# Optimization experiments

Measured on AMD Instinct MI355X. Metric: run time of the kernel, lower is better.

## Reference

```python
import jax, jax.numpy as jnp
import numpy as np

B, T, I, H = 64, 1024, 128, 256

def setup_inputs() -> dict:
    key = jax.random.key(0)
    ks = jax.random.split(key, 9)
    std = 1.0 / np.sqrt(H)
    u = lambda k, shape: jax.random.uniform(k, shape, jnp.float32, -std, std)
    return {
        "x": jax.random.normal(ks[0], (B, T, I), jnp.float32),
        # layer 0: concat dim = I + H
        "Wf1": u(ks[1], (I + H, H)), "bf1": u(ks[2], (H,)),
        "Wc1": u(ks[3], (I + H, H)), "bc1": u(ks[4], (H,)),
        # layer 1: concat dim = H + H
        "Wf2": u(ks[5], (H + H, H)), "bf2": u(ks[6], (H,)),
        "Wc2": u(ks[7], (H + H, H)), "bc2": u(ks[8], (H,)),
    }

def _mgu_layer(x_seq, Wf, bf, Wc, bc):
    # x_seq: [B, T, D] -> outputs [B, T, H], final hidden [B, H]
    h0 = jnp.zeros((x_seq.shape[0], H), x_seq.dtype)
    def step(h, x_t):
        comb = jnp.concatenate([x_t, h], axis=-1)      # [B, D+H]
        f = jax.nn.sigmoid(comb @ Wf + bf)             # forget gate
        c = jnp.tanh(comb @ Wc + bc)                   # candidate
        h_new = f * h + (1.0 - f) * c
        return h_new, h_new
    hT, ys = jax.lax.scan(step, h0, jnp.swapaxes(x_seq, 0, 1))  # ys: [T, B, H]
    return jnp.swapaxes(ys, 0, 1), hT

def reference(x, Wf1, bf1, Wc1, bc1, Wf2, bf2, Wc2, bc2):
    y1, h1 = _mgu_layer(x, Wf1, bf1, Wc1, bc1)
    y2, h2 = _mgu_layer(y1, Wf2, bf2, Wc2, bc2)
    hidden = jnp.stack([h1, h2])  # [num_layers, B, H]
    return y2, hidden
```

## Files before the change

### kernel.cpp

```cpp
#include <hip/hip_runtime.h>

typedef unsigned int uint;
typedef _Float16 f16;
typedef _Float16 f16x2 __attribute__((ext_vector_type(2)));
typedef _Float16 f16x4 __attribute__((ext_vector_type(4)));
typedef _Float16 f16x8 __attribute__((ext_vector_type(8)));
typedef float f32x4 __attribute__((ext_vector_type(4)));

#define B_ 64
#define T_ 1024
#define I_ 128
#define H_ 256

template<int KIN>
__global__ void prep_wxt(const float* __restrict__ Wf, const float* __restrict__ Wc,
                         f16* __restrict__ WxT) {
  int o = blockIdx.x * 256 + threadIdx.x;
  if (o >= 512 * KIN) return;
  int n = o / KIN, k = o % KIN;
  float v = (n < 256) ? Wf[k * H_ + n] : Wc[k * H_ + (n - 256)];
  WxT[o] = (f16)v;
}

__global__ void prep_ut(const float* __restrict__ Wf, const float* __restrict__ Wc,
                        f16* __restrict__ UT, int DIN) {
  int o = blockIdx.x * 256 + threadIdx.x;
  int n = o >> 8, k = o & 255;
  const float* W = (n < 256) ? Wf : Wc;
  UT[o] = (f16)W[(DIN + k) * H_ + (n & 255)];
}

__global__ void init_sync(int* s) { if (threadIdx.x < 132) s[threadIdx.x] = 0; }

template<int KFULL, bool AF32>
__global__ __launch_bounds__(256) void gemm_xpart(const void* __restrict__ Av,
    const f16* __restrict__ Bt, const float* __restrict__ bf, const float* __restrict__ bc,
    f16* __restrict__ Xg) {
  __shared__ __align__(16) f16 As[128][72];
  __shared__ __align__(16) f16 Bs[128][72];
  const int m0 = blockIdx.x * 128, n0 = blockIdx.y * 128;
  const int tid = threadIdx.x, lane = tid & 63, wid = tid >> 6;
  const int wr = wid >> 1, wc = wid & 1;
  f32x4 zero4 = {0.f, 0.f, 0.f, 0.f};
  f32x4 acc[4][4];
  #pragma unroll
  for (int i = 0; i < 4; ++i)
    #pragma unroll
    for (int j = 0; j < 4; ++j) acc[i][j] = zero4;
  const int r2 = tid >> 1, hh = tid & 1;
  for (int kb = 0; kb < KFULL / 64; ++kb) {
    const int k0 = kb * 64;
    if (kb) __syncthreads();
    if (AF32) {
      const float* A = (const float*)Av;
      const float* src = A + (size_t)(m0 + r2) * KFULL + k0 + hh * 32;
      #pragma unroll
      for (int i = 0; i < 8; ++i) {
        float4 v = *(const float4*)(src + i * 4);
        f16x4 p = { (f16)v.x, (f16)v.y, (f16)v.z, (f16)v.w };
        *(f16x4*)&As[r2][hh * 32 + i * 4] = p;
      }
    } else {
      const f16* A = (const f16*)Av;
      const f16* src = A + (size_t)(m0 + r2) * KFULL + k0 + hh * 32;
      #pragma unroll
      for (int i = 0; i < 4; ++i)
        *(uint4*)&As[r2][hh * 32 + i * 8] = *(const uint4*)(src + i * 8);
    }
    {
      const f16* src = Bt + (size_t)(n0 + r2) * KFULL + k0 + hh * 32;
      #pragma unroll
      for (int i = 0; i < 4; ++i)
        *(uint4*)&Bs[r2][hh * 32 + i * 8] = *(const uint4*)(src + i * 8);
    }
    __syncthreads();
    #pragma unroll
    for (int kt = 0; kt < 2; ++kt) {
      f16x8 af[4], bfr[4];
      #pragma unroll
      for (int i = 0; i < 4; ++i)
        af[i] = *(const f16x8*)&As[wr * 64 + i * 16 + (lane & 15)][kt * 32 + (lane >> 4) * 8];
      #pragma unroll
      for (int j = 0; j < 4; ++j)
        bfr[j] = *(const f16x8*)&Bs[wc * 64 + j * 16 + (lane & 15)][kt * 32 + (lane >> 4) * 8];
      #pragma unroll
      for (int i = 0; i < 4; ++i)
        #pragma unroll
        for (int j = 0; j < 4; ++j)
          acc[i][j] = __builtin_amdgcn_mfma_f32_16x16x32_f16(af[i], bfr[j], acc[i][j], 0, 0, 0);
    }
  }
  const float* bias = (n0 < 256) ? bf : bc;
  #pragma unroll
  for (int j = 0; j < 4; ++j) {
    const int gn = n0 + wc * 64 + j * 16 + (lane & 15);
    const float bv = bias[gn & 255];
    #pragma unroll
    for (int i = 0; i < 4; ++i) {
      #pragma unroll
      for (int reg = 0; reg < 4; ++reg) {
        const int gm = m0 + wr * 64 + i * 16 + (lane >> 4) * 4 + reg;
        Xg[(size_t)gm * 512 + gn] = (f16)(acc[i][j][reg] + bv);
      }
    }
  }
}

__device__ __forceinline__ void gemm_tile_l2(const f16* __restrict__ A,
    const f16* __restrict__ Bt, const float* __restrict__ bf, const float* __restrict__ bc,
    f16* __restrict__ Xg, int m0, int n0, f16 (*As)[72], f16 (*Bs)[72]) {
  const int tid = threadIdx.x, lane = tid & 63, wid = tid >> 6;
  const bool act = tid < 256;
  f32x4 zero4 = {0.f, 0.f, 0.f, 0.f};
  f32x4 acc[2][2];
  #pragma unroll
  for (int i = 0; i < 2; ++i)
    #pragma unroll
    for (int j = 0; j < 2; ++j) acc[i][j] = zero4;
  const int arow = tid >> 3, aq = tid & 7;
  const int r2 = (tid & 255) >> 1, hh = tid & 1;
  for (int kb = 0; kb < 4; ++kb) {
    const int k0 = kb * 64;
    if (kb) __syncthreads();
    if (act) {
      const f16* srcA = A + (size_t)(m0 + arow) * 256 + k0 + aq * 8;
      *(uint4*)&As[arow][aq * 8] = *(const uint4*)srcA;
      const f16* srcB = Bt + (size_t)(n0 + r2) * 256 + k0 + hh * 32;
      #pragma unroll
      for (int i = 0; i < 4; ++i)
        *(uint4*)&Bs[r2][hh * 32 + i * 8] = *(const uint4*)(srcB + i * 8);
    }
    __syncthreads();
    if (wid < 4) {
      #pragma unroll
      for (int kt = 0; kt < 2; ++kt) {
        f16x8 af[2], bfr[2];
        #pragma unroll
        for (int i = 0; i < 2; ++i)
          af[i] = *(const f16x8*)&As[i * 16 + (lane & 15)][kt * 32 + (lane >> 4) * 8];
        #pragma unroll
        for (int j = 0; j < 2; ++j)
          bfr[j] = *(const f16x8*)&Bs[wid * 32 + j * 16 + (lane & 15)][kt * 32 + (lane >> 4) * 8];
        #pragma unroll
        for (int i = 0; i < 2; ++i)
          #pragma unroll
          for (int j = 0; j < 2; ++j)
            acc[i][j] = __builtin_amdgcn_mfma_f32_16x16x32_f16(af[i], bfr[j], acc[i][j], 0, 0, 0);
      }
    }
  }
  if (wid < 4) {
    const float* bias = (n0 < 256) ? bf : bc;
    #pragma unroll
    for (int j = 0; j < 2; ++j) {
      const int gn = n0 + wid * 32 + j * 16 + (lane & 15);
      const float bv = bias[gn & 255];
      #pragma unroll
      for (int i = 0; i < 2; ++i) {
        #pragma unroll
        for (int reg = 0; reg < 4; ++reg) {
          const int gm = m0 + i * 16 + (lane >> 4) * 4 + reg;
          Xg[(size_t)gm * 512 + gn] = (f16)(acc[i][j][reg] + bv);
        }
      }
    }
  }
  __syncthreads();
}

__device__ __forceinline__ void rec_core(const f16* __restrict__ UT,
    f16* __restrict__ Xg, float* __restrict__ yf, f16* __restrict__ yh,
    float* __restrict__ hid, const int g, int* prog_pub, int* done_gate,
    f16 (*hbuf)[16][264]) {
  const int tid = threadIdx.x;
  const int lane = tid & 63, w = tid >> 6;
  const int lr = lane & 15, lg = lane >> 4;
  const int m0 = g * 16;

  const int nt[4] = { 32 * w, 32 * w + 16, 256 + 32 * w, 256 + 32 * w + 16 };

  f16x8 uw[4][8];
  #pragma unroll
  for (int tt = 0; tt < 4; ++tt)
    #pragma unroll
    for (int kf = 0; kf < 8; ++kf)
      uw[tt][kf] = *(const f16x8*)&UT[(size_t)(nt[tt] + lr) * 256 + kf * 32 + lg * 8];
  #pragma unroll
  for (int tt = 0; tt < 4; ++tt)
    #pragma unroll
    for (int kf = 0; kf < 8; ++kf)
      asm volatile("" : "+v"(uw[tt][kf]));

  {
    uint* hz = (uint*)&hbuf[0][0][0];
    for (int i = tid; i < 2112; i += 512) hz[i] = 0u;
  }

  if (done_gate) {
    if (tid == 0)
      while (__hip_atomic_load(&done_gate[0], __ATOMIC_ACQUIRE, __HIP_MEMORY_SCOPE_AGENT) < 64)
        __builtin_amdgcn_s_sleep(8);
    __syncthreads();
  }

  const f16* xp[4];
  #pragma unroll
  for (int tt = 0; tt < 4; ++tt)
    xp[tt] = Xg + ((size_t)(m0 + lr) * T_) * 512 + nt[tt] + 4 * lg;

  float hreg[2][4] = {{0.f,0.f,0.f,0.f},{0.f,0.f,0.f,0.f}};
  f16x4 xcur[4];
  #pragma unroll
  for (int tt = 0; tt < 4; ++tt) xcur[tt] = *(const f16x4*)xp[tt];

  const size_t ybase = (size_t)(m0 + lr) * T_ * H_;
  const int ycol0 = 32 * w + 4 * lg;

  __syncthreads();

  #pragma unroll 1
  for (int t = 0; t < T_; ++t) {
    if (done_gate) {
      const int tp1 = t + 1;
      if ((tp1 & 31) == 0 && (tp1 >> 5) < 32) {
        if (tid == 0)
          while (__hip_atomic_load(&done_gate[tp1 >> 5], __ATOMIC_ACQUIRE, __HIP_MEMORY_SCOPE_AGENT) < 64)
            __builtin_amdgcn_s_sleep(8);
        __syncthreads();
      }
    }

    const int tn = (t + 1 < T_) ? t + 1 : t;
    f16x4 xn[4];
    #pragma unroll
    for (int tt = 0; tt < 4; ++tt) xn[tt] = *(const f16x4*)(xp[tt] + (size_t)tn * 512);

    const f16* hrow = &hbuf[t & 1][lr][0];
    f16x8 hf[8];
    #pragma unroll
    for (int kf = 0; kf < 8; ++kf)
      hf[kf] = *(const f16x8*)(hrow + kf * 32 + lg * 8);

    f32x4 acc[4];
    #pragma unroll
    for (int tt = 0; tt < 4; ++tt) acc[tt] = (f32x4){0.f, 0.f, 0.f, 0.f};
    #pragma unroll
    for (int kf = 0; kf < 8; ++kf)
      #pragma unroll
      for (int tt = 0; tt < 4; ++tt)
        acc[tt] = __builtin_amdgcn_mfma_f32_16x16x32_f16(uw[tt][kf], hf[kf], acc[tt], 0, 0, 0);

    f16x4 hn4[2];
    #pragma unroll
    for (int p = 0; p < 2; ++p) {
      #pragma unroll
      for (int r = 0; r < 4; ++r) {
        float pf = acc[p][r]     + (float)xcur[p][r];
        float pc = acc[2 + p][r] + (float)xcur[2 + p][r];
        float fg = __builtin_amdgcn_rcpf(1.f + __expf(-pf));
        float e2 = __expf(2.f * pc);
        float cc = 1.f - 2.f * __builtin_amdgcn_rcpf(e2 + 1.f);
        float hn = cc + fg * (hreg[p][r] - cc);
        hreg[p][r] = hn;
        hn4[p][r] = (f16)hn;
      }
      *(f16x4*)&hbuf[(t + 1) & 1][lr][ycol0 + 16 * p] = hn4[p];
    }
    if (yh) {
      #pragma unroll
      for (int p = 0; p < 2; ++p)
        *(f16x4*)(yh + ybase + (size_t)t * H_ + ycol0 + 16 * p) = hn4[p];
    }
    if (yf) {
      #pragma unroll
      for (int p = 0; p < 2; ++p) {
        float4 yv = make_float4(hreg[p][0], hreg[p][1], hreg[p][2], hreg[p][3]);
        *(float4*)(yf + ybase + (size_t)t * H_ + ycol0 + 16 * p) = yv;
      }
    }
    if (t == T_ - 1) {
      #pragma unroll
      for (int p = 0; p < 2; ++p) {
        float4 hv = make_float4(hreg[p][0], hreg[p][1], hreg[p][2], hreg[p][3]);
        *(float4*)(hid + (size_t)(m0 + lr) * H_ + ycol0 + 16 * p) = hv;
      }
    }

    asm volatile("s_waitcnt lgkmcnt(0)" ::: "memory");
    __builtin_amdgcn_s_barrier();
    asm volatile("" ::: "memory");

    if (prog_pub && ((t & 31) == 31)) {
      asm volatile("s_waitcnt vmcnt(0)" ::: "memory");
      __syncthreads();
      if (tid == 0)
        __hip_atomic_store(prog_pub, t + 1, __ATOMIC_RELEASE, __HIP_MEMORY_SCOPE_AGENT);
    }

    #pragma unroll
    for (int tt = 0; tt < 4; ++tt) xcur[tt] = xn[tt];
  }
}

__global__ __launch_bounds__(512, 1) void fused(const f16* __restrict__ UT1,
    const f16* __restrict__ UT2, f16* __restrict__ Xg, const f16* __restrict__ Wx2T,
    const float* __restrict__ bf2, const float* __restrict__ bc2,
    f16* __restrict__ y1h, float* __restrict__ y2,
    float* __restrict__ hid1, float* __restrict__ hid2, int* __restrict__ sync) {
  __shared__ __align__(16) f16 hbuf[2][16][264];
  __shared__ __align__(16) f16 As[32][72];
  __shared__ __align__(16) f16 Bs[128][72];
  int* prog = sync;
  int* done = sync + 4;
  const int bid = blockIdx.x, tid = threadIdx.x;

  if (bid < 4) {
    rec_core(UT1, Xg, nullptr, y1h, hid1, bid, &prog[bid], nullptr, hbuf);
  } else if (bid < 68) {
    const int wk = bid - 4;
    for (int j = 0; j < 128; ++j) {
      const int tau = wk + 64 * j;
      const int c = tau >> 8, rem = tau & 255, b = rem >> 2, n = rem & 3;
      const int g1 = b >> 4;
      if (tid == 0)
        while (__hip_atomic_load(&prog[g1], __ATOMIC_ACQUIRE, __HIP_MEMORY_SCOPE_AGENT) < c * 32 + 32)
          __builtin_amdgcn_s_sleep(8);
      __syncthreads();
      gemm_tile_l2(y1h, Wx2T, bf2, bc2, Xg, b * 1024 + c * 32, n * 128, As, Bs);
      asm volatile("s_waitcnt vmcnt(0)" ::: "memory");
      __syncthreads();
      if (tid == 0)
        __hip_atomic_fetch_add(&done[g1 * 32 + c], 1, __ATOMIC_ACQ_REL, __HIP_MEMORY_SCOPE_AGENT);
    }
  } else {
    const int g = bid - 68;
    rec_core(UT2, Xg, y2, nullptr, hid2, g, nullptr, &done[g * 32], hbuf);
  }
}

extern "C" void kernel_launch(void* const* d_in, const int* in_sizes, int n_in,
                              void* d_out, int out_size, void* d_ws, size_t ws_size,
                              hipStream_t stream) {
  (void)in_sizes; (void)n_in; (void)out_size; (void)ws_size;
  const float* x   = (const float*)d_in[0];
  const float* Wf1 = (const float*)d_in[1];
  const float* bf1 = (const float*)d_in[2];
  const float* Wc1 = (const float*)d_in[3];
  const float* bc1 = (const float*)d_in[4];
  const float* Wf2 = (const float*)d_in[5];
  const float* bf2 = (const float*)d_in[6];
  const float* Wc2 = (const float*)d_in[7];
  const float* bc2 = (const float*)d_in[8];
  float* out = (float*)d_out;

  char* ws = (char*)d_ws;
  f16*  Xg   = (f16*)(ws);
  f16*  y1h  = (f16*)(ws + 67108864);
  f16*  Wx1T = (f16*)(ws + 100663296);
  f16*  Wx2T = (f16*)(ws + 100794368);
  f16*  UT1  = (f16*)(ws + 101056512);
  f16*  UT2  = (f16*)(ws + 101318656);
  int*  sync = (int*)(ws + 101580800);

  float* y2   = out;
  float* hid1 = out + (size_t)B_ * T_ * H_;
  float* hid2 = hid1 + (size_t)B_ * H_;

  prep_wxt<128><<<256, 256, 0, stream>>>(Wf1, Wc1, Wx1T);
  prep_wxt<256><<<512, 256, 0, stream>>>(Wf2, Wc2, Wx2T);
  prep_ut<<<512, 256, 0, stream>>>(Wf1, Wc1, UT1, 128);
  prep_ut<<<512, 256, 0, stream>>>(Wf2, Wc2, UT2, 256);
  init_sync<<<1, 256, 0, stream>>>(sync);

  gemm_xpart<128, true ><<<dim3(512, 4), 256, 0, stream>>>(x, Wx1T, bf1, bc1, Xg);
  fused<<<72, 512, 0, stream>>>(UT1, UT2, Xg, Wx2T, bf2, bc2, y1h, y2, hid1, hid2, sync);
}
```

Measured before the change: 1.795 ms.

## Fold weight prep and layer-1 input GEMM into the persistent fused kernel

```diff
diff --git a/kernel.cpp b/kernel.cpp
--- a/kernel.cpp
+++ b/kernel.cpp
@@ -2,7 +2,6 @@
 
 typedef unsigned int uint;
 typedef _Float16 f16;
-typedef _Float16 f16x2 __attribute__((ext_vector_type(2)));
 typedef _Float16 f16x4 __attribute__((ext_vector_type(4)));
 typedef _Float16 f16x8 __attribute__((ext_vector_type(8)));
 typedef float f32x4 __attribute__((ext_vector_type(4)));
@@ -11,102 +10,10 @@
 #define T_ 1024
 #define I_ 128
 #define H_ 256
-
-template<int KIN>
-__global__ void prep_wxt(const float* __restrict__ Wf, const float* __restrict__ Wc,
-                         f16* __restrict__ WxT) {
-  int o = blockIdx.x * 256 + threadIdx.x;
-  if (o >= 512 * KIN) return;
-  int n = o / KIN, k = o % KIN;
-  float v = (n < 256) ? Wf[k * H_ + n] : Wc[k * H_ + (n - 256)];
-  WxT[o] = (f16)v;
-}
-
-__global__ void prep_ut(const float* __restrict__ Wf, const float* __restrict__ Wc,
-                        f16* __restrict__ UT, int DIN) {
-  int o = blockIdx.x * 256 + threadIdx.x;
-  int n = o >> 8, k = o & 255;
-  const float* W = (n < 256) ? Wf : Wc;
-  UT[o] = (f16)W[(DIN + k) * H_ + (n & 255)];
-}
-
-__global__ void init_sync(int* s) { if (threadIdx.x < 132) s[threadIdx.x] = 0; }
-
-template<int KFULL, bool AF32>
-__global__ __launch_bounds__(256) void gemm_xpart(const void* __restrict__ Av,
-    const f16* __restrict__ Bt, const float* __restrict__ bf, const float* __restrict__ bc,
-    f16* __restrict__ Xg) {
-  __shared__ __align__(16) f16 As[128][72];
-  __shared__ __align__(16) f16 Bs[128][72];
-  const int m0 = blockIdx.x * 128, n0 = blockIdx.y * 128;
-  const int tid = threadIdx.x, lane = tid & 63, wid = tid >> 6;
-  const int wr = wid >> 1, wc = wid & 1;
-  f32x4 zero4 = {0.f, 0.f, 0.f, 0.f};
-  f32x4 acc[4][4];
-  #pragma unroll
-  for (int i = 0; i < 4; ++i)
-    #pragma unroll
-    for (int j = 0; j < 4; ++j) acc[i][j] = zero4;
-  const int r2 = tid >> 1, hh = tid & 1;
-  for (int kb = 0; kb < KFULL / 64; ++kb) {
-    const int k0 = kb * 64;
-    if (kb) __syncthreads();
-    if (AF32) {
-      const float* A = (const float*)Av;
-      const float* src = A + (size_t)(m0 + r2) * KFULL + k0 + hh * 32;
-      #pragma unroll
-      for (int i = 0; i < 8; ++i) {
-        float4 v = *(const float4*)(src + i * 4);
-        f16x4 p = { (f16)v.x, (f16)v.y, (f16)v.z, (f16)v.w };
-        *(f16x4*)&As[r2][hh * 32 + i * 4] = p;
-      }
-    } else {
-      const f16* A = (const f16*)Av;
-      const f16* src = A + (size_t)(m0 + r2) * KFULL + k0 + hh * 32;
-      #pragma unroll
-      for (int i = 0; i < 4; ++i)
-        *(uint4*)&As[r2][hh * 32 + i * 8] = *(const uint4*)(src + i * 8);
-    }
-    {
-      const f16* src = Bt + (size_t)(n0 + r2) * KFULL + k0 + hh * 32;
-      #pragma unroll
-      for (int i = 0; i < 4; ++i)
-        *(uint4*)&Bs[r2][hh * 32 + i * 8] = *(const uint4*)(src + i * 8);
-    }
-    __syncthreads();
-    #pragma unroll
-    for (int kt = 0; kt < 2; ++kt) {
-      f16x8 af[4], bfr[4];
-      #pragma unroll
-      for (int i = 0; i < 4; ++i)
-        af[i] = *(const f16x8*)&As[wr * 64 + i * 16 + (lane & 15)][kt * 32 + (lane >> 4) * 8];
-      #pragma unroll
-      for (int j = 0; j < 4; ++j)
-        bfr[j] = *(const f16x8*)&Bs[wc * 64 + j * 16 + (lane & 15)][kt * 32 + (lane >> 4) * 8];
-      #pragma unroll
-      for (int i = 0; i < 4; ++i)
-        #pragma unroll
-        for (int j = 0; j < 4; ++j)
-          acc[i][j] = __builtin_amdgcn_mfma_f32_16x16x32_f16(af[i], bfr[j], acc[i][j], 0, 0, 0);
-    }
-  }
-  const float* bias = (n0 < 256) ? bf : bc;
-  #pragma unroll
-  for (int j = 0; j < 4; ++j) {
-    const int gn = n0 + wc * 64 + j * 16 + (lane & 15);
-    const float bv = bias[gn & 255];
-    #pragma unroll
-    for (int i = 0; i < 4; ++i) {
-      #pragma unroll
-      for (int reg = 0; reg < 4; ++reg) {
-        const int gm = m0 + wr * 64 + i * 16 + (lane >> 4) * 4 + reg;
-        Xg[(size_t)gm * 512 + gn] = (f16)(acc[i][j][reg] + bv);
-      }
-    }
-  }
-}
-
-__device__ __forceinline__ void gemm_tile_l2(const f16* __restrict__ A,
+#define NWK 64
+
+template<int KA, bool AF32>
+__device__ __forceinline__ void gemm_tile(const void* __restrict__ Av,
     const f16* __restrict__ Bt, const float* __restrict__ bf, const float* __restrict__ bc,
     f16* __restrict__ Xg, int m0, int n0, f16 (*As)[72], f16 (*Bs)[72]) {
   const int tid = threadIdx.x, lane = tid & 63, wid = tid >> 6;
@@ -119,13 +26,22 @@
     for (int j = 0; j < 2; ++j) acc[i][j] = zero4;
   const int arow = tid >> 3, aq = tid & 7;
   const int r2 = (tid & 255) >> 1, hh = tid & 1;
-  for (int kb = 0; kb < 4; ++kb) {
+  for (int kb = 0; kb < KA / 64; ++kb) {
     const int k0 = kb * 64;
     if (kb) __syncthreads();
     if (act) {
-      const f16* srcA = A + (size_t)(m0 + arow) * 256 + k0 + aq * 8;
-      *(uint4*)&As[arow][aq * 8] = *(const uint4*)srcA;
-      const f16* srcB = Bt + (size_t)(n0 + r2) * 256 + k0 + hh * 32;
+      if (AF32) {
+        const float* srcA = (const float*)Av + (size_t)(m0 + arow) * KA + k0 + aq * 8;
+        float4 v0 = *(const float4*)srcA;
+        float4 v1 = *(const float4*)(srcA + 4);
+        f16x8 p = { (f16)v0.x, (f16)v0.y, (f16)v0.z, (f16)v0.w,
+                    (f16)v1.x, (f16)v1.y, (f16)v1.z, (f16)v1.w };
+        *(f16x8*)&As[arow][aq * 8] = p;
+      } else {
+        const f16* srcA = (const f16*)Av + (size_t)(m0 + arow) * KA + k0 + aq * 8;
+        *(uint4*)&As[arow][aq * 8] = *(const uint4*)srcA;
+      }
+      const f16* srcB = Bt + (size_t)(n0 + r2) * KA + k0 + hh * 32;
       #pragma unroll
       for (int i = 0; i < 4; ++i)
         *(uint4*)&Bs[r2][hh * 32 + i * 8] = *(const uint4*)(srcB + i * 8);
@@ -168,10 +84,11 @@
   __syncthreads();
 }
 
-__device__ __forceinline__ void rec_core(const f16* __restrict__ UT,
+__device__ __forceinline__ void rec_core(const float* __restrict__ Wf,
+    const float* __restrict__ Wc, const int DIN,
     f16* __restrict__ Xg, float* __restrict__ yf, f16* __restrict__ yh,
     float* __restrict__ hid, const int g, int* prog_pub, int* done_gate,
-    f16 (*hbuf)[16][264]) {
+    const int start_chunk, f16 (*hbuf)[16][264]) {
   const int tid = threadIdx.x;
   const int lane = tid & 63, w = tid >> 6;
   const int lr = lane & 15, lg = lane >> 4;
@@ -181,10 +98,18 @@
 
   f16x8 uw[4][8];
   #pragma unroll
-  for (int tt = 0; tt < 4; ++tt)
-    #pragma unroll
-    for (int kf = 0; kf < 8; ++kf)
-      uw[tt][kf] = *(const f16x8*)&UT[(size_t)(nt[tt] + lr) * 256 + kf * 32 + lg * 8];
+  for (int tt = 0; tt < 4; ++tt) {
+    const float* Wsel = (nt[tt] < 256) ? Wf : Wc;
+    const int col = (nt[tt] & 255) + lr;
+    #pragma unroll
+    for (int kf = 0; kf < 8; ++kf) {
+      __align__(16) f16 tmp[8];
+      #pragma unroll
+      for (int j = 0; j < 8; ++j)
+        tmp[j] = (f16)Wsel[(size_t)(DIN + kf * 32 + lg * 8 + j) * 256 + col];
+      uw[tt][kf] = *(const f16x8*)tmp;
+    }
+  }
   #pragma unroll
   for (int tt = 0; tt < 4; ++tt)
     #pragma unroll
@@ -196,12 +121,10 @@
     for (int i = tid; i < 2112; i += 512) hz[i] = 0u;
   }
 
-  if (done_gate) {
-    if (tid == 0)
-      while (__hip_atomic_load(&done_gate[0], __ATOMIC_ACQUIRE, __HIP_MEMORY_SCOPE_AGENT) < 64)
-        __builtin_amdgcn_s_sleep(8);
-    __syncthreads();
-  }
+  if (tid == 0)
+    while (__hip_atomic_load(&done_gate[start_chunk], __ATOMIC_ACQUIRE, __HIP_MEMORY_SCOPE_AGENT) < 64)
+      __builtin_amdgcn_s_sleep(8);
+  __syncthreads();
 
   const f16* xp[4];
   #pragma unroll
@@ -220,7 +143,7 @@
 
   #pragma unroll 1
   for (int t = 0; t < T_; ++t) {
-    if (done_gate) {
+    {
       const int tp1 = t + 1;
       if ((tp1 & 31) == 0 && (tp1 >> 5) < 32) {
         if (tid == 0)
@@ -302,39 +225,98 @@
   }
 }
 
-__global__ __launch_bounds__(512, 1) void fused(const f16* __restrict__ UT1,
-    const f16* __restrict__ UT2, f16* __restrict__ Xg, const f16* __restrict__ Wx2T,
-    const float* __restrict__ bf2, const float* __restrict__ bc2,
+__device__ __forceinline__ void worker(const int wk, const float* __restrict__ x,
+    const float* __restrict__ Wf1, const float* __restrict__ bf1,
+    const float* __restrict__ Wc1, const float* __restrict__ bc1,
+    const float* __restrict__ Wf2, const float* __restrict__ bf2,
+    const float* __restrict__ Wc2, const float* __restrict__ bc2,
+    f16* __restrict__ Wx1T, f16* __restrict__ Wx2T,
+    const f16* __restrict__ y1h, f16* __restrict__ Xg,
+    int* prep_done, int* prog, int* done1, int* done2,
+    f16 (*As)[72], f16 (*Bs)[72]) {
+  const int tid = threadIdx.x;
+
+  for (int i = tid; i < 3072; i += 512) {
+    const int o = wk * 3072 + i;
+    if (o < 65536) {
+      const int n = o >> 7, k = o & 127;
+      Wx1T[o] = (f16)(((n < 256) ? Wf1 : Wc1)[k * 256 + (n & 255)]);
+    } else {
+      const int o2 = o - 65536;
+      const int n = o2 >> 8, k = o2 & 255;
+      Wx2T[o2] = (f16)(((n < 256) ? Wf2 : Wc2)[k * 256 + (n & 255)]);
+    }
+  }
+  asm volatile("s_waitcnt vmcnt(0)" ::: "memory");
+  __syncthreads();
+  if (tid == 0) {
+    __hip_atomic_fetch_add(prep_done, 1, __ATOMIC_ACQ_REL, __HIP_MEMORY_SCOPE_AGENT);
+    while (__hip_atomic_load(prep_done, __ATOMIC_ACQUIRE, __HIP_MEMORY_SCOPE_AGENT) < NWK)
+      __builtin_amdgcn_s_sleep(2);
+  }
+  __syncthreads();
+
+  #pragma unroll 1
+  for (int c = 0; c < 32; ++c) {
+    if (c < 16) {
+      #pragma unroll 1
+      for (int cc = 2 * c; cc <= 2 * c + 1; ++cc) {
+        #pragma unroll 1
+        for (int s = 0; s < 4; ++s) {
+          const int rem = (wk + 64 * s) & 255;
+          const int b = rem >> 2, n = rem & 3, g1 = b >> 4;
+          gemm_tile<128, true>(x, Wx1T, bf1, bc1, Xg, b * 1024 + cc * 32, n * 128, As, Bs);
+          asm volatile("s_waitcnt vmcnt(0)" ::: "memory");
+          __syncthreads();
+          if (tid == 0)
+            __hip_atomic_fetch_add(&done1[g1 * 32 + cc], 1, __ATOMIC_ACQ_REL, __HIP_MEMORY_SCOPE_AGENT);
+        }
+      }
+    }
+    #pragma unroll 1
+    for (int s = 0; s < 4; ++s) {
+      const int rem = (wk + 64 * s) & 255;
+      const int b = rem >> 2, n = rem & 3, g1 = b >> 4;
+      if (tid == 0)
+        while (__hip_atomic_load(&prog[g1], __ATOMIC_ACQUIRE, __HIP_MEMORY_SCOPE_AGENT) < c * 32 + 32)
+          __builtin_amdgcn_s_sleep(8);
+      __syncthreads();
+      gemm_tile<256, false>(y1h, Wx2T, bf2, bc2, Xg, b * 1024 + c * 32, n * 128, As, Bs);
+      asm volatile("s_waitcnt vmcnt(0)" ::: "memory");
+      __syncthreads();
+      if (tid == 0)
+        __hip_atomic_fetch_add(&done2[g1 * 32 + c], 1, __ATOMIC_ACQ_REL, __HIP_MEMORY_SCOPE_AGENT);
+    }
+  }
+}
+
+__global__ __launch_bounds__(512, 1) void fused(const float* __restrict__ x,
+    const float* __restrict__ Wf1, const float* __restrict__ bf1,
+    const float* __restrict__ Wc1, const float* __restrict__ bc1,
+    const float* __restrict__ Wf2, const float* __restrict__ bf2,
+    const float* __restrict__ Wc2, const float* __restrict__ bc2,
+    f16* __restrict__ Xg, f16* __restrict__ Wx1T, f16* __restrict__ Wx2T,
     f16* __restrict__ y1h, float* __restrict__ y2,
     float* __restrict__ hid1, float* __restrict__ hid2, int* __restrict__ sync) {
   __shared__ __align__(16) f16 hbuf[2][16][264];
   __shared__ __align__(16) f16 As[32][72];
   __shared__ __align__(16) f16 Bs[128][72];
-  int* prog = sync;
-  int* done = sync + 4;
-  const int bid = blockIdx.x, tid = threadIdx.x;
+  int* prep_done = sync;
+  int* prog  = sync + 1;
+  int* done1 = sync + 5;
+  int* done2 = sync + 133;
+  const int bid = blockIdx.x;
 
   if (bid < 4) {
-    rec_core(UT1, Xg, nullptr, y1h, hid1, bid, &prog[bid], nullptr, hbuf);
+    rec_core(Wf1, Wc1, 128, Xg, nullptr, y1h, hid1, bid,
+             &prog[bid], &done1[bid * 32], 0, hbuf);
   } else if (bid < 68) {
-    const int wk = bid - 4;
-    for (int j = 0; j < 128; ++j) {
-      const int tau = wk + 64 * j;
-      const int c = tau >> 8, rem = tau & 255, b = rem >> 2, n = rem & 3;
-      const int g1 = b >> 4;
-      if (tid == 0)
-        while (__hip_atomic_load(&prog[g1], __ATOMIC_ACQUIRE, __HIP_MEMORY_SCOPE_AGENT) < c * 32 + 32)
-          __builtin_amdgcn_s_sleep(8);
-      __syncthreads();
-      gemm_tile_l2(y1h, Wx2T, bf2, bc2, Xg, b * 1024 + c * 32, n * 128, As, Bs);
-      asm volatile("s_waitcnt vmcnt(0)" ::: "memory");
-      __syncthreads();
-      if (tid == 0)
-        __hip_atomic_fetch_add(&done[g1 * 32 + c], 1, __ATOMIC_ACQ_REL, __HIP_MEMORY_SCOPE_AGENT);
-    }
+    worker(bid - 4, x, Wf1, bf1, Wc1, bc1, Wf2, bf2, Wc2, bc2,
+           Wx1T, Wx2T, y1h, Xg, prep_done, prog, done1, done2, As, Bs);
   } else {
     const int g = bid - 68;
-    rec_core(UT2, Xg, y2, nullptr, hid2, g, nullptr, &done[g * 32], hbuf);
+    rec_core(Wf2, Wc2, 256, Xg, y2, nullptr, hid2, g,
+             nullptr, &done2[g * 32], 1, hbuf);
   }
 }
 
@@ -358,20 +340,13 @@
   f16*  y1h  = (f16*)(ws + 67108864);
   f16*  Wx1T = (f16*)(ws + 100663296);
   f16*  Wx2T = (f16*)(ws + 100794368);
-  f16*  UT1  = (f16*)(ws + 101056512);
-  f16*  UT2  = (f16*)(ws + 101318656);
-  int*  sync = (int*)(ws + 101580800);
+  int*  sync = (int*)(ws + 101056512);
 
   float* y2   = out;
   float* hid1 = out + (size_t)B_ * T_ * H_;
   float* hid2 = hid1 + (size_t)B_ * H_;
 
-  prep_wxt<128><<<256, 256, 0, stream>>>(Wf1, Wc1, Wx1T);
-  prep_wxt<256><<<512, 256, 0, stream>>>(Wf2, Wc2, Wx2T);
-  prep_ut<<<512, 256, 0, stream>>>(Wf1, Wc1, UT1, 128);
-  prep_ut<<<512, 256, 0, stream>>>(Wf2, Wc2, UT2, 256);
-  init_sync<<<1, 256, 0, stream>>>(sync);
-
-  gemm_xpart<128, true ><<<dim3(512, 4), 256, 0, stream>>>(x, Wx1T, bf1, bc1, Xg);
-  fused<<<72, 512, 0, stream>>>(UT1, UT2, Xg, Wx2T, bf2, bc2, y1h, y2, hid1, hid2, sync);
-}
+  hipMemsetAsync(sync, 0, 261 * sizeof(int), stream);
+  fused<<<72, 512, 0, stream>>>(x, Wf1, bf1, Wc1, bc1, Wf2, bf2, Wc2, bc2,
+                                Xg, Wx1T, Wx2T, y1h, y2, hid1, hid2, sync);
+}
```

Result: slower. 1.860 ms (+3.6%).
